# Optimization experiments

Hardware: AMD Instinct MI355X
Metric: run time of the kernel (lower is better)

The kernel has to match this reference:

```python
import jax, jax.numpy as jnp
import numpy as np

N_HEADS = 16


def setup_inputs() -> dict:
    key = jax.random.key(0)
    ks = jax.random.split(key, 5)
    B, T, C = 4, 2048, 1024
    x = jax.random.normal(ks[0], (B, T, C), dtype=jnp.float32)
    w_qkv = jax.random.normal(ks[1], (C, 3 * C), dtype=jnp.float32) * (1.0 / np.sqrt(C))
    b_qkv = jnp.zeros((3 * C,), dtype=jnp.float32)
    w_proj = jax.random.normal(ks[2], (C, C), dtype=jnp.float32) * (1.0 / np.sqrt(C))
    b_proj = jnp.zeros((C,), dtype=jnp.float32)
    return {"x": x, "w_qkv": w_qkv, "b_qkv": b_qkv, "w_proj": w_proj, "b_proj": b_proj}


def reference(x, w_qkv, b_qkv, w_proj, b_proj):
    B, T, C = x.shape
    H = N_HEADS
    D = C // H
    scale = 1.0 / np.sqrt(D).astype(np.float32)
    qkv = x @ w_qkv + b_qkv                      # [B,T,3C]
    qkv = qkv.reshape(B, T, 3, H, D)
    q, k, v = [jnp.transpose(qkv[:, :, i], (0, 2, 1, 3)) for i in range(3)]  # [B,H,T,D]
    attn = jnp.einsum('bhqd,bhkd->bhqk', q, k) * scale
    causal = jnp.tril(jnp.ones((T, T), dtype=bool))
    attn = jnp.where(causal[None, None], attn, -jnp.inf)
    attn = jax.nn.softmax(attn, axis=-1)
    out = jnp.einsum('bhqk,bhkd->bhqd', attn, v)  # [B,H,T,D]
    out = jnp.transpose(out, (0, 2, 1, 3)).reshape(B, T, C)
    return out @ w_proj + b_proj
```

## Files before the change

kernel.cpp:

```cpp
#include <hip/hip_runtime.h>
#include <cstdint>

typedef unsigned short u16;
typedef uint32_t u32;
typedef __attribute__((ext_vector_type(8))) short bf16x8;
typedef __attribute__((ext_vector_type(4))) short bf16x4;
typedef __attribute__((ext_vector_type(4))) float f32x4;

#define NB 4
#define NT 2048
#define NC 1024
#define NH 16
#define ND 64
#define NM (NB*NT)
#define N3C (3*NC)
#define NQT (NT/64)

#define QSCALE 0.18033688011112042f

static __device__ __forceinline__ u16 f2bf(float f){
  union { float f; uint32_t u; } v; v.f = f;
  return (u16)((v.u + 0x7fffu + ((v.u >> 16) & 1u)) >> 16);
}

static __device__ __forceinline__ void gld_lds16(void* lds, const void* g){
  auto lp = reinterpret_cast<__attribute__((address_space(3))) uint32_t*>(
      reinterpret_cast<uintptr_t>(lds));
  auto gp = reinterpret_cast<__attribute__((address_space(1))) uint32_t*>(
      reinterpret_cast<uintptr_t>(g));
  __builtin_amdgcn_global_load_lds(gp, lp, 16, 0, 0);
}

static __device__ __forceinline__ f32x4 mfma16(bf16x4 a, bf16x4 b, f32x4 c){
#if __has_builtin(__builtin_amdgcn_mfma_f32_16x16x16bf16_1k)
  return __builtin_amdgcn_mfma_f32_16x16x16bf16_1k(a, b, c, 0, 0, 0);
#else
  asm("v_mfma_f32_16x16x16_bf16 %0, %1, %2, %0" : "+v"(c) : "v"(a), "v"(b));
  return c;
#endif
}

__global__ __launch_bounds__(256) void k_cast(const float* __restrict__ in,
                                              u16* __restrict__ out){
  const int i = (blockIdx.x * 256 + threadIdx.x) * 4;
  const float4 vv = *reinterpret_cast<const float4*>(in + i);
  union { u16 s[4]; uint64_t u; } pk;
  pk.s[0] = f2bf(vv.x); pk.s[1] = f2bf(vv.y);
  pk.s[2] = f2bf(vv.z); pk.s[3] = f2bf(vv.w);
  *reinterpret_cast<uint64_t*>(out + i) = pk.u;
}

__global__ __launch_bounds__(256) void k_transpose_cast(const float* __restrict__ in,
                                                        u16* __restrict__ out,
                                                        int R, int Cc){
  __shared__ float tile[32][33];
  const int bx = blockIdx.x * 32, by = blockIdx.y * 32;
  const int tx = threadIdx.x, ty = threadIdx.y;
#pragma unroll
  for (int i = 0; i < 32; i += 8)
    tile[ty + i][tx] = in[(size_t)(by + ty + i) * Cc + bx + tx];
  __syncthreads();
#pragma unroll
  for (int i = 0; i < 32; i += 8)
    out[(size_t)(bx + ty + i) * R + by + tx] = f2bf(tile[tx][ty + i]);
}

static __device__ __forceinline__ void gemm_mainloop(
    const u16* __restrict__ A, const u16* __restrict__ Bt, int K,
    int m0, int n0, u16* As, u16* Bs, f32x4 acc[4][4])
{
  const int tid = threadIdx.x;
  const int wave = tid >> 6, lane = tid & 63;
  const int wm = wave >> 1, wn = wave & 1;
  const int o0 = tid * 8, o1 = o0 + 2048;
  const u16* Ag0 = A  + (size_t)(m0 + (o0 >> 5)) * K + (o0 & 31);
  const u16* Ag1 = A  + (size_t)(m0 + (o1 >> 5)) * K + (o1 & 31);
  const u16* Bg0 = Bt + (size_t)(n0 + (o0 >> 5)) * K + (o0 & 31);
  const u16* Bg1 = Bt + (size_t)(n0 + (o1 >> 5)) * K + (o1 & 31);
  u16* AsW = As + wave * 512;
  u16* BsW = Bs + wave * 512;
  const int kb = (lane >> 4) * 8, rl = lane & 15;

  for (int kt = 0; kt < K; kt += 32){
    gld_lds16(AsW,        Ag0 + kt);
    gld_lds16(AsW + 2048, Ag1 + kt);
    gld_lds16(BsW,        Bg0 + kt);
    gld_lds16(BsW + 2048, Bg1 + kt);
    __syncthreads();
    bf16x8 af[4], bfr[4];
#pragma unroll
    for (int i = 0; i < 4; i++){
      af[i]  = *reinterpret_cast<const bf16x8*>(&As[(wm * 64 + i * 16 + rl) * 32 + kb]);
      bfr[i] = *reinterpret_cast<const bf16x8*>(&Bs[(wn * 64 + i * 16 + rl) * 32 + kb]);
    }
#pragma unroll
    for (int i = 0; i < 4; i++)
#pragma unroll
      for (int j = 0; j < 4; j++)
        acc[i][j] = __builtin_amdgcn_mfma_f32_16x16x32_bf16(af[i], bfr[j], acc[i][j], 0, 0, 0);
    __syncthreads();
  }
}

__global__ __launch_bounds__(256) void k_gemm_qkv(
    const u16* __restrict__ A, const u16* __restrict__ Bt,
    const float* __restrict__ bias,
    u16* __restrict__ qo, u16* __restrict__ ko, u16* __restrict__ vo)
{
  __shared__ u16 As[128 * 32], Bs[128 * 32];
  f32x4 acc[4][4] = {};
  const int m0 = blockIdx.y * 128, n0 = blockIdx.x * 128;
  gemm_mainloop(A, Bt, NC, m0, n0, As, Bs, acc);

  const int tid = threadIdx.x;
  const int wave = tid >> 6, lane = tid & 63;
  const int wm = wave >> 1, wn = wave & 1;
  const int rl = lane & 15, rg = lane >> 4;
  const int which = n0 >> 10;
  if (which == 2){
#pragma unroll
    for (int j = 0; j < 4; j++){
      const int n = n0 + wn * 64 + j * 16 + rl;
      const int cc = n & 1023;
      const int h = cc >> 6, d = cc & 63;
      const float bb = bias[n];
#pragma unroll
      for (int i = 0; i < 4; i++){
        const int mb = m0 + wm * 64 + i * 16 + rg * 4;
        const int b = mb >> 11, t0 = mb & 2047;
        const size_t bhb = ((size_t)(b * NH + h)) * NT * ND;
        union { u16 s[4]; uint64_t u; } pk4;
#pragma unroll
        for (int r = 0; r < 4; r++) pk4.s[r] = f2bf(acc[i][j][r] + bb);
        *reinterpret_cast<uint64_t*>(
          &vo[bhb + (size_t)(t0 >> 6) * 4096 + d * 64 + ((((t0 >> 2) & 15) ^ (d & 7)) << 2)]) = pk4.u;
      }
    }
  } else {
#pragma unroll
    for (int j = 0; j < 4; j++){
      const int n = n0 + wn * 64 + j * 16 + rl;
      const int cc = n & 1023;
      const int h = cc >> 6, d = cc & 63;
      const float bb = bias[n];
#pragma unroll
      for (int i = 0; i < 4; i++){
#pragma unroll
        for (int r = 0; r < 4; r++){
          const int m = m0 + wm * 64 + i * 16 + rg * 4 + r;
          const int b = m >> 11, t = m & 2047;
          const size_t bhb = ((size_t)(b * NH + h)) * NT * ND;
          const float val = acc[i][j][r] + bb;
          if (which == 0){
            qo[bhb + (size_t)t * ND + d] = f2bf(val * QSCALE);
          } else {
            ko[bhb + (size_t)(t >> 6) * 4096 + (t & 63) * 64 + (d ^ ((t & 7) << 3))] = f2bf(val);
          }
        }
      }
    }
  }
}

__global__ __launch_bounds__(256) void k_gemm_proj(
    const u16* __restrict__ A, const u16* __restrict__ Bt,
    const float* __restrict__ bias, float* __restrict__ out)
{
  __shared__ u16 As[128 * 32], Bs[128 * 32];
  f32x4 acc[4][4] = {};
  const int m0 = blockIdx.y * 128, n0 = blockIdx.x * 128;
  gemm_mainloop(A, Bt, NC, m0, n0, As, Bs, acc);

  const int tid = threadIdx.x;
  const int wave = tid >> 6, lane = tid & 63;
  const int wm = wave >> 1, wn = wave & 1;
  const int rl = lane & 15, rg = lane >> 4;
#pragma unroll
  for (int i = 0; i < 4; i++){
#pragma unroll
    for (int r = 0; r < 4; r++){
      const int m = m0 + wm * 64 + i * 16 + rg * 4 + r;
#pragma unroll
      for (int j = 0; j < 4; j++){
        const int n = n0 + wn * 64 + j * 16 + rl;
        out[(size_t)m * NC + n] = acc[i][j][r] + bias[n];
      }
    }
  }
}

static __device__ __forceinline__ void flash_one(
    int qt, const u16* __restrict__ q, const u16* __restrict__ kb,
    const u16* __restrict__ vb, u16* __restrict__ ao, int bh,
    u16 (*Ks)[4096], u16 (*Vt)[4096])
{
  const int tid = threadIdx.x, wave = tid >> 6, lane = tid & 63;
  const int cl = lane & 15, g = lane >> 4;
  const int c0 = wave * 2;
  const size_t base = (size_t)bh * NT * ND;
  const u16* kg0 = kb + base;
  const u16* vg0 = vb + base;

  bf16x8 qf0, qf1;
  {
    const u16* qrow = q + base + (size_t)(qt * 64 + wave * 16 + cl) * ND;
    qf0 = *reinterpret_cast<const bf16x8*>(qrow + g * 8);
    qf1 = *reinterpret_cast<const bf16x8*>(qrow + 32 + g * 8);
  }
  asm volatile("" : "+v"(qf0), "+v"(qf1));

  f32x4 o[4] = {};
  float mrun = -1e30f, lrun = 0.f;
  const int n = qt + 1;

  gld_lds16(&Ks[0][(c0    ) * 512], kg0 + (c0    ) * 512 + lane * 8);
  gld_lds16(&Ks[0][(c0 + 1) * 512], kg0 + (c0 + 1) * 512 + lane * 8);
  gld_lds16(&Vt[0][(c0    ) * 512], vg0 + (c0    ) * 512 + lane * 8);
  gld_lds16(&Vt[0][(c0 + 1) * 512], vg0 + (c0 + 1) * 512 + lane * 8);

  for (int t = 0; t < n; ++t){
    const int cur = t & 1, nxt = cur ^ 1;
    if (t + 1 < n){
      const u16* kg = kg0 + (size_t)(t + 1) * 4096;
      const u16* vg = vg0 + (size_t)(t + 1) * 4096;
      gld_lds16(&Ks[nxt][(c0    ) * 512], kg + (c0    ) * 512 + lane * 8);
      gld_lds16(&Ks[nxt][(c0 + 1) * 512], kg + (c0 + 1) * 512 + lane * 8);
      gld_lds16(&Vt[nxt][(c0    ) * 512], vg + (c0    ) * 512 + lane * 8);
      gld_lds16(&Vt[nxt][(c0 + 1) * 512], vg + (c0 + 1) * 512 + lane * 8);
      asm volatile("s_waitcnt vmcnt(4)" ::: "memory");
    } else {
      asm volatile("s_waitcnt vmcnt(0)" ::: "memory");
    }
    __builtin_amdgcn_sched_barrier(0);
    __builtin_amdgcn_s_barrier();

    const u16* KsC = Ks[cur];
    const u16* VtC = Vt[cur];
    f32x4 s[4];
    __builtin_amdgcn_s_setprio(1);
#pragma unroll
    for (int nf = 0; nf < 4; nf++){
      const int kj = nf * 16 + cl;
      const u16* krow = &KsC[kj * 64];
      const bf16x8 kf0 = *reinterpret_cast<const bf16x8*>(&krow[((0 + g) ^ (kj & 7)) * 8]);
      const bf16x8 kf1 = *reinterpret_cast<const bf16x8*>(&krow[((4 + g) ^ (kj & 7)) * 8]);
      f32x4 a = {};
      a = __builtin_amdgcn_mfma_f32_16x16x32_bf16(kf0, qf0, a, 0, 0, 0);
      a = __builtin_amdgcn_mfma_f32_16x16x32_bf16(kf1, qf1, a, 0, 0, 0);
      s[nf] = a;
    }
    __builtin_amdgcn_s_setprio(0);

    if (t == qt){
      const int qrl = wave * 16 + cl;
#pragma unroll
      for (int nf = 0; nf < 4; nf++)
#pragma unroll
        for (int r = 0; r < 4; r++)
          if (nf * 16 + g * 4 + r > qrl) s[nf][r] = -3e38f;
    }

    float rmax = -3e38f;
#pragma unroll
    for (int nf = 0; nf < 4; nf++)
#pragma unroll
      for (int r = 0; r < 4; r++) rmax = fmaxf(rmax, s[nf][r]);
    rmax = fmaxf(rmax, __shfl_xor(rmax, 16));
    rmax = fmaxf(rmax, __shfl_xor(rmax, 32));
    const float mnew = fmaxf(mrun, rmax);
    const float alpha = exp2f(mrun - mnew);
    mrun = mnew;
    float rs = 0.f;
#pragma unroll
    for (int nf = 0; nf < 4; nf++)
#pragma unroll
      for (int r = 0; r < 4; r++){
        s[nf][r] = exp2f(s[nf][r] - mnew);
        rs += s[nf][r];
      }
    rs += __shfl_xor(rs, 16);
    rs += __shfl_xor(rs, 32);
    lrun = lrun * alpha + rs;

    const float a0 = __shfl(alpha, g * 4 + 0);
    const float a1 = __shfl(alpha, g * 4 + 1);
    const float a2 = __shfl(alpha, g * 4 + 2);
    const float a3 = __shfl(alpha, g * 4 + 3);
#pragma unroll
    for (int fo = 0; fo < 4; fo++){
      o[fo][0] *= a0; o[fo][1] *= a1; o[fo][2] *= a2; o[fo][3] *= a3;
    }

    u32 pk[4][2];
#pragma unroll
    for (int nf = 0; nf < 4; nf++){
      asm("v_cvt_pk_bf16_f32 %0, %1, %2" : "=v"(pk[nf][0]) : "v"(s[nf][0]), "v"(s[nf][1]));
      asm("v_cvt_pk_bf16_f32 %0, %1, %2" : "=v"(pk[nf][1]) : "v"(s[nf][2]), "v"(s[nf][3]));
    }

    __builtin_amdgcn_s_setprio(1);
#pragma unroll
    for (int nf = 0; nf < 4; nf++){
      union { u32 u[2]; bf16x4 v; } pa;
      pa.u[0] = pk[nf][0]; pa.u[1] = pk[nf][1];
#pragma unroll
      for (int fo = 0; fo < 4; fo++){
        const int d = fo * 16 + cl;
        const bf16x4 vf = *reinterpret_cast<const bf16x4*>(
            &VtC[d * 64 + (((nf * 4 + g) ^ (d & 7)) << 2)]);
        o[fo] = mfma16(pa.v, vf, o[fo]);
      }
    }
    __builtin_amdgcn_s_setprio(0);

    asm volatile("s_waitcnt lgkmcnt(0)" ::: "memory");
    __builtin_amdgcn_sched_barrier(0);
    __builtin_amdgcn_s_barrier();
  }

  float linv[4];
#pragma unroll
  for (int r = 0; r < 4; r++) linv[r] = 1.0f / __shfl(lrun, g * 4 + r);
  const int b = bh >> 4, h = bh & 15;
#pragma unroll
  for (int fo = 0; fo < 4; fo++){
#pragma unroll
    for (int r = 0; r < 4; r++){
      const int t = qt * 64 + wave * 16 + g * 4 + r;
      const int c = h * 64 + fo * 16 + cl;
      ao[((size_t)b * NT + t) * NC + c] = f2bf(o[fo][r] * linv[r]);
    }
  }
}

__global__ __launch_bounds__(256) void k_flash(
    const u16* __restrict__ q, const u16* __restrict__ k,
    const u16* __restrict__ v, u16* __restrict__ ao)
{
  __shared__ u16 Ks[2][4096];
  __shared__ u16 Vt[2][4096];
  const int px = blockIdx.x, bh = blockIdx.y;
  flash_one(px,           q, k, v, ao, bh, Ks, Vt);
  __builtin_amdgcn_s_barrier();
  flash_one(NQT - 1 - px, q, k, v, ao, bh, Ks, Vt);
}

extern "C" void kernel_launch(void* const* d_in, const int* in_sizes, int n_in,
                              void* d_out, int out_size, void* d_ws, size_t ws_size,
                              hipStream_t stream){
  const float* x      = (const float*)d_in[0];
  const float* w_qkv  = (const float*)d_in[1];
  const float* b_qkv  = (const float*)d_in[2];
  const float* w_proj = (const float*)d_in[3];
  const float* b_proj = (const float*)d_in[4];
  float* out = (float*)d_out;

  u16* ws = (u16*)d_ws;
  u16* xb     = ws;
  u16* qb     = ws + 8388608;
  u16* kb     = ws + 16777216;
  u16* vb     = ws + 25165824;
  u16* aob    = ws + 33554432;
  u16* wqkvT  = ws + 41943040;
  u16* wprojT = ws + 45088768;

  k_cast<<<8388608 / 1024, 256, 0, stream>>>(x, xb);
  k_transpose_cast<<<dim3(N3C / 32, NC / 32), dim3(32, 8), 0, stream>>>(w_qkv, wqkvT, NC, N3C);
  k_transpose_cast<<<dim3(NC / 32, NC / 32), dim3(32, 8), 0, stream>>>(w_proj, wprojT, NC, NC);
  k_gemm_qkv<<<dim3(N3C / 128, NM / 128), 256, 0, stream>>>(xb, wqkvT, b_qkv, qb, kb, vb);
  k_flash<<<dim3(NQT / 2, NB * NH), 256, 0, stream>>>(qb, kb, vb, aob);
  k_gemm_proj<<<dim3(NC / 128, NM / 128), 256, 0, stream>>>(aob, wprojT, b_proj, out);
}
```

Measured before the change: 228.7 us.

## Process paired query tiles in one KV sweep and skip rescale when max stable

Each flash block previously handled its two causal-balanced query tiles in two separate passes over K/V. Now both tiles share a single pass: each K/V chunk is loaded into LDS once and used for both query tiles, the shorter tile stopping at its diagonal. This removes the duplicated K/V global loads and barriers. The softmax also skips the alpha rescale of the output accumulator unless the running max grows by more than a threshold, a lazy-rescale trick that trades a small numeric-range margin for fewer multiplies. Holding two sets of accumulators raises register pressure, which may lower occupancy.

```diff
diff --git a/kernel.cpp b/kernel.cpp
--- a/kernel.cpp
+++ b/kernel.cpp
@@ -189,38 +189,131 @@
   }
 }
 
-static __device__ __forceinline__ void flash_one(
-    int qt, const u16* __restrict__ q, const u16* __restrict__ kb,
-    const u16* __restrict__ vb, u16* __restrict__ ao, int bh,
-    u16 (*Ks)[4096], u16 (*Vt)[4096])
-{
+static __device__ __forceinline__ void qkt(const u16* __restrict__ KsC,
+                                           bf16x8 qf0, bf16x8 qf1,
+                                           int cl, int g, f32x4 s[4])
+{
+  __builtin_amdgcn_s_setprio(1);
+#pragma unroll
+  for (int nf = 0; nf < 4; nf++){
+    const int kj = nf * 16 + cl;
+    const u16* krow = &KsC[kj * 64];
+    const bf16x8 kf0 = *reinterpret_cast<const bf16x8*>(&krow[((0 + g) ^ (kj & 7)) * 8]);
+    const bf16x8 kf1 = *reinterpret_cast<const bf16x8*>(&krow[((4 + g) ^ (kj & 7)) * 8]);
+    f32x4 a = {};
+    a = __builtin_amdgcn_mfma_f32_16x16x32_bf16(kf0, qf0, a, 0, 0, 0);
+    a = __builtin_amdgcn_mfma_f32_16x16x32_bf16(kf1, qf1, a, 0, 0, 0);
+    s[nf] = a;
+  }
+  __builtin_amdgcn_s_setprio(0);
+}
+
+static __device__ __forceinline__ void maskdiag(f32x4 s[4], int wave, int cl, int g){
+  const int qrl = wave * 16 + cl;
+#pragma unroll
+  for (int nf = 0; nf < 4; nf++)
+#pragma unroll
+    for (int r = 0; r < 4; r++)
+      if (nf * 16 + g * 4 + r > qrl) s[nf][r] = -3e38f;
+}
+
+static __device__ __forceinline__ void sm_pv(
+    f32x4 s[4], f32x4 o[4], float& mrun, float& lrun,
+    const u16* __restrict__ VtC, int cl, int g)
+{
+  float rmax = -3e38f;
+#pragma unroll
+  for (int nf = 0; nf < 4; nf++)
+#pragma unroll
+    for (int r = 0; r < 4; r++) rmax = fmaxf(rmax, s[nf][r]);
+  rmax = fmaxf(rmax, __shfl_xor(rmax, 16));
+  rmax = fmaxf(rmax, __shfl_xor(rmax, 32));
+  if (!__all(rmax <= mrun + 8.0f)){
+    const float mnew = fmaxf(mrun, rmax);
+    const float alpha = exp2f(mrun - mnew);
+    mrun = mnew;
+    lrun *= alpha;
+    const float a0 = __shfl(alpha, g * 4 + 0);
+    const float a1 = __shfl(alpha, g * 4 + 1);
+    const float a2 = __shfl(alpha, g * 4 + 2);
+    const float a3 = __shfl(alpha, g * 4 + 3);
+#pragma unroll
+    for (int fo = 0; fo < 4; fo++){
+      o[fo][0] *= a0; o[fo][1] *= a1; o[fo][2] *= a2; o[fo][3] *= a3;
+    }
+  }
+  float rs = 0.f;
+#pragma unroll
+  for (int nf = 0; nf < 4; nf++)
+#pragma unroll
+    for (int r = 0; r < 4; r++){
+      s[nf][r] = exp2f(s[nf][r] - mrun);
+      rs += s[nf][r];
+    }
+  rs += __shfl_xor(rs, 16);
+  rs += __shfl_xor(rs, 32);
+  lrun += rs;
+
+  u32 pk[4][2];
+#pragma unroll
+  for (int nf = 0; nf < 4; nf++){
+    asm("v_cvt_pk_bf16_f32 %0, %1, %2" : "=v"(pk[nf][0]) : "v"(s[nf][0]), "v"(s[nf][1]));
+    asm("v_cvt_pk_bf16_f32 %0, %1, %2" : "=v"(pk[nf][1]) : "v"(s[nf][2]), "v"(s[nf][3]));
+  }
+  __builtin_amdgcn_s_setprio(1);
+#pragma unroll
+  for (int nf = 0; nf < 4; nf++){
+    union { u32 u[2]; bf16x4 v; } pa;
+    pa.u[0] = pk[nf][0]; pa.u[1] = pk[nf][1];
+#pragma unroll
+    for (int fo = 0; fo < 4; fo++){
+      const int d = fo * 16 + cl;
+      const bf16x4 vf = *reinterpret_cast<const bf16x4*>(
+          &VtC[d * 64 + (((nf * 4 + g) ^ (d & 7)) << 2)]);
+      o[fo] = mfma16(pa.v, vf, o[fo]);
+    }
+  }
+  __builtin_amdgcn_s_setprio(0);
+}
+
+__global__ __launch_bounds__(256) void k_flash(
+    const u16* __restrict__ q, const u16* __restrict__ k,
+    const u16* __restrict__ v, u16* __restrict__ ao)
+{
+  __shared__ u16 Ks[2][4096];
+  __shared__ u16 Vt[2][4096];
   const int tid = threadIdx.x, wave = tid >> 6, lane = tid & 63;
   const int cl = lane & 15, g = lane >> 4;
   const int c0 = wave * 2;
+  const int px = blockIdx.x, bh = blockIdx.y;
+  const int qt1 = px, qt2 = NQT - 1 - px;
+  const int ntot = qt2 + 1;
   const size_t base = (size_t)bh * NT * ND;
-  const u16* kg0 = kb + base;
-  const u16* vg0 = vb + base;
-
-  bf16x8 qf0, qf1;
+  const u16* kg0 = k + base;
+  const u16* vg0 = v + base;
+
+  bf16x8 q1f0, q1f1, q2f0, q2f1;
   {
-    const u16* qrow = q + base + (size_t)(qt * 64 + wave * 16 + cl) * ND;
-    qf0 = *reinterpret_cast<const bf16x8*>(qrow + g * 8);
-    qf1 = *reinterpret_cast<const bf16x8*>(qrow + 32 + g * 8);
-  }
-  asm volatile("" : "+v"(qf0), "+v"(qf1));
-
-  f32x4 o[4] = {};
-  float mrun = -1e30f, lrun = 0.f;
-  const int n = qt + 1;
+    const u16* qr1 = q + base + (size_t)(qt1 * 64 + wave * 16 + cl) * ND;
+    q1f0 = *reinterpret_cast<const bf16x8*>(qr1 + g * 8);
+    q1f1 = *reinterpret_cast<const bf16x8*>(qr1 + 32 + g * 8);
+    const u16* qr2 = q + base + (size_t)(qt2 * 64 + wave * 16 + cl) * ND;
+    q2f0 = *reinterpret_cast<const bf16x8*>(qr2 + g * 8);
+    q2f1 = *reinterpret_cast<const bf16x8*>(qr2 + 32 + g * 8);
+  }
+  asm volatile("" : "+v"(q1f0), "+v"(q1f1), "+v"(q2f0), "+v"(q2f1));
+
+  f32x4 o1[4] = {}, o2[4] = {};
+  float m1 = -1e30f, l1 = 0.f, m2 = -1e30f, l2 = 0.f;
 
   gld_lds16(&Ks[0][(c0    ) * 512], kg0 + (c0    ) * 512 + lane * 8);
   gld_lds16(&Ks[0][(c0 + 1) * 512], kg0 + (c0 + 1) * 512 + lane * 8);
   gld_lds16(&Vt[0][(c0    ) * 512], vg0 + (c0    ) * 512 + lane * 8);
   gld_lds16(&Vt[0][(c0 + 1) * 512], vg0 + (c0 + 1) * 512 + lane * 8);
 
-  for (int t = 0; t < n; ++t){
+  for (int t = 0; t < ntot; ++t){
     const int cur = t & 1, nxt = cur ^ 1;
-    if (t + 1 < n){
+    if (t + 1 < ntot){
       const u16* kg = kg0 + (size_t)(t + 1) * 4096;
       const u16* vg = vg0 + (size_t)(t + 1) * 4096;
       gld_lds16(&Ks[nxt][(c0    ) * 512], kg + (c0    ) * 512 + lane * 8);
@@ -236,113 +329,43 @@
 
     const u16* KsC = Ks[cur];
     const u16* VtC = Vt[cur];
-    f32x4 s[4];
-    __builtin_amdgcn_s_setprio(1);
-#pragma unroll
-    for (int nf = 0; nf < 4; nf++){
-      const int kj = nf * 16 + cl;
-      const u16* krow = &KsC[kj * 64];
-      const bf16x8 kf0 = *reinterpret_cast<const bf16x8*>(&krow[((0 + g) ^ (kj & 7)) * 8]);
-      const bf16x8 kf1 = *reinterpret_cast<const bf16x8*>(&krow[((4 + g) ^ (kj & 7)) * 8]);
-      f32x4 a = {};
-      a = __builtin_amdgcn_mfma_f32_16x16x32_bf16(kf0, qf0, a, 0, 0, 0);
-      a = __builtin_amdgcn_mfma_f32_16x16x32_bf16(kf1, qf1, a, 0, 0, 0);
-      s[nf] = a;
-    }
-    __builtin_amdgcn_s_setprio(0);
-
-    if (t == qt){
-      const int qrl = wave * 16 + cl;
-#pragma unroll
-      for (int nf = 0; nf < 4; nf++)
-#pragma unroll
-        for (int r = 0; r < 4; r++)
-          if (nf * 16 + g * 4 + r > qrl) s[nf][r] = -3e38f;
-    }
-
-    float rmax = -3e38f;
-#pragma unroll
-    for (int nf = 0; nf < 4; nf++)
-#pragma unroll
-      for (int r = 0; r < 4; r++) rmax = fmaxf(rmax, s[nf][r]);
-    rmax = fmaxf(rmax, __shfl_xor(rmax, 16));
-    rmax = fmaxf(rmax, __shfl_xor(rmax, 32));
-    const float mnew = fmaxf(mrun, rmax);
-    const float alpha = exp2f(mrun - mnew);
-    mrun = mnew;
-    float rs = 0.f;
-#pragma unroll
-    for (int nf = 0; nf < 4; nf++)
-#pragma unroll
-      for (int r = 0; r < 4; r++){
-        s[nf][r] = exp2f(s[nf][r] - mnew);
-        rs += s[nf][r];
-      }
-    rs += __shfl_xor(rs, 16);
-    rs += __shfl_xor(rs, 32);
-    lrun = lrun * alpha + rs;
-
-    const float a0 = __shfl(alpha, g * 4 + 0);
-    const float a1 = __shfl(alpha, g * 4 + 1);
-    const float a2 = __shfl(alpha, g * 4 + 2);
-    const float a3 = __shfl(alpha, g * 4 + 3);
-#pragma unroll
-    for (int fo = 0; fo < 4; fo++){
-      o[fo][0] *= a0; o[fo][1] *= a1; o[fo][2] *= a2; o[fo][3] *= a3;
-    }
-
-    u32 pk[4][2];
-#pragma unroll
-    for (int nf = 0; nf < 4; nf++){
-      asm("v_cvt_pk_bf16_f32 %0, %1, %2" : "=v"(pk[nf][0]) : "v"(s[nf][0]), "v"(s[nf][1]));
-      asm("v_cvt_pk_bf16_f32 %0, %1, %2" : "=v"(pk[nf][1]) : "v"(s[nf][2]), "v"(s[nf][3]));
-    }
-
-    __builtin_amdgcn_s_setprio(1);
-#pragma unroll
-    for (int nf = 0; nf < 4; nf++){
-      union { u32 u[2]; bf16x4 v; } pa;
-      pa.u[0] = pk[nf][0]; pa.u[1] = pk[nf][1];
-#pragma unroll
-      for (int fo = 0; fo < 4; fo++){
-        const int d = fo * 16 + cl;
-        const bf16x4 vf = *reinterpret_cast<const bf16x4*>(
-            &VtC[d * 64 + (((nf * 4 + g) ^ (d & 7)) << 2)]);
-        o[fo] = mfma16(pa.v, vf, o[fo]);
-      }
-    }
-    __builtin_amdgcn_s_setprio(0);
+
+    {
+      f32x4 s[4];
+      qkt(KsC, q2f0, q2f1, cl, g, s);
+      if (t == qt2) maskdiag(s, wave, cl, g);
+      sm_pv(s, o2, m2, l2, VtC, cl, g);
+    }
+    if (t <= qt1){
+      f32x4 s[4];
+      qkt(KsC, q1f0, q1f1, cl, g, s);
+      if (t == qt1) maskdiag(s, wave, cl, g);
+      sm_pv(s, o1, m1, l1, VtC, cl, g);
+    }
 
     asm volatile("s_waitcnt lgkmcnt(0)" ::: "memory");
     __builtin_amdgcn_sched_barrier(0);
     __builtin_amdgcn_s_barrier();
   }
 
-  float linv[4];
-#pragma unroll
-  for (int r = 0; r < 4; r++) linv[r] = 1.0f / __shfl(lrun, g * 4 + r);
+  float li1[4], li2[4];
+#pragma unroll
+  for (int r = 0; r < 4; r++){
+    li1[r] = 1.0f / __shfl(l1, g * 4 + r);
+    li2[r] = 1.0f / __shfl(l2, g * 4 + r);
+  }
   const int b = bh >> 4, h = bh & 15;
 #pragma unroll
   for (int fo = 0; fo < 4; fo++){
 #pragma unroll
     for (int r = 0; r < 4; r++){
-      const int t = qt * 64 + wave * 16 + g * 4 + r;
       const int c = h * 64 + fo * 16 + cl;
-      ao[((size_t)b * NT + t) * NC + c] = f2bf(o[fo][r] * linv[r]);
-    }
-  }
-}
-
-__global__ __launch_bounds__(256) void k_flash(
-    const u16* __restrict__ q, const u16* __restrict__ k,
-    const u16* __restrict__ v, u16* __restrict__ ao)
-{
-  __shared__ u16 Ks[2][4096];
-  __shared__ u16 Vt[2][4096];
-  const int px = blockIdx.x, bh = blockIdx.y;
-  flash_one(px,           q, k, v, ao, bh, Ks, Vt);
-  __builtin_amdgcn_s_barrier();
-  flash_one(NQT - 1 - px, q, k, v, ao, bh, Ks, Vt);
+      const int t1 = qt1 * 64 + wave * 16 + g * 4 + r;
+      ao[((size_t)b * NT + t1) * NC + c] = f2bf(o1[fo][r] * li1[r]);
+      const int t2 = qt2 * 64 + wave * 16 + g * 4 + r;
+      ao[((size_t)b * NT + t2) * NC + c] = f2bf(o2[fo][r] * li2[r]);
+    }
+  }
 }
 
 extern "C" void kernel_launch(void* const* d_in, const int* in_sizes, int n_in,
```

After: 223.2 us. -2.4%, faster.

## Rewrite flash attention with 32x32 MFMA, shared KV stream for paired query tiles

Applied to the files above, without the earlier changes.

The flash kernel moves from 16x16 MFMA tiles to 32x32x16 bf16 MFMA, with each wave owning 32 query rows. Each block now processes its two causal-balanced 128-row query blocks together while streaming a single K/V pass, so K/V tiles staged into LDS are reused by both query sets. The V layout written by the QKV GEMM changes to an 8-element swizzle to match the new fragment loads. It also adds permlane32 swaps to build the P operand and a lazy rescale that skips the alpha correction unless the row max grows by more than 8. The trade-off is higher register pressure from two sets of accumulators and Q fragments, and a grid halved to 8x64 blocks.

```diff
diff --git a/kernel.cpp b/kernel.cpp
--- a/kernel.cpp
+++ b/kernel.cpp
@@ -4,8 +4,8 @@
 typedef unsigned short u16;
 typedef uint32_t u32;
 typedef __attribute__((ext_vector_type(8))) short bf16x8;
-typedef __attribute__((ext_vector_type(4))) short bf16x4;
 typedef __attribute__((ext_vector_type(4))) float f32x4;
+typedef __attribute__((ext_vector_type(16))) float f32x16;
 
 #define NB 4
 #define NT 2048
@@ -14,7 +14,6 @@
 #define ND 64
 #define NM (NB*NT)
 #define N3C (3*NC)
-#define NQT (NT/64)
 
 #define QSCALE 0.18033688011112042f
 
@@ -31,13 +30,8 @@
   __builtin_amdgcn_global_load_lds(gp, lp, 16, 0, 0);
 }
 
-static __device__ __forceinline__ f32x4 mfma16(bf16x4 a, bf16x4 b, f32x4 c){
-#if __has_builtin(__builtin_amdgcn_mfma_f32_16x16x16bf16_1k)
-  return __builtin_amdgcn_mfma_f32_16x16x16bf16_1k(a, b, c, 0, 0, 0);
-#else
-  asm("v_mfma_f32_16x16x16_bf16 %0, %1, %2, %0" : "+v"(c) : "v"(a), "v"(b));
-  return c;
-#endif
+static __device__ __forceinline__ f32x16 mfma32(bf16x8 a, bf16x8 b, f32x16 c){
+  return __builtin_amdgcn_mfma_f32_32x32x16_bf16(a, b, c, 0, 0, 0);
 }
 
 __global__ __launch_bounds__(256) void k_cast(const float* __restrict__ in,
@@ -133,7 +127,8 @@
 #pragma unroll
         for (int r = 0; r < 4; r++) pk4.s[r] = f2bf(acc[i][j][r] + bb);
         *reinterpret_cast<uint64_t*>(
-          &vo[bhb + (size_t)(t0 >> 6) * 4096 + d * 64 + ((((t0 >> 2) & 15) ^ (d & 7)) << 2)]) = pk4.u;
+          &vo[bhb + (size_t)(t0 >> 6) * 4096 + d * 64 +
+              ((((t0 >> 3) & 7) ^ (d & 7)) << 3) + (t0 & 7)]) = pk4.u;
       }
     }
   } else {
@@ -189,44 +184,160 @@
   }
 }
 
-static __device__ __forceinline__ void flash_one(
-    int qt, const u16* __restrict__ q, const u16* __restrict__ kb,
-    const u16* __restrict__ vb, u16* __restrict__ ao, int bh,
-    u16 (*Ks)[4096], u16 (*Vt)[4096])
-{
+static __device__ __forceinline__ void upd32(
+    const u16* __restrict__ Kc, const u16* __restrict__ Vc,
+    const bf16x8* qf, f32x16& o0, f32x16& o1,
+    float& mrun, float& lrun, int kbase, int qglob, bool domask,
+    int hi, int l31, int l7)
+{
+  f32x16 s0 = {}, s1 = {};
+  __builtin_amdgcn_s_setprio(1);
+#pragma unroll
+  for (int ds = 0; ds < 4; ds++){
+    const int sw = ((ds * 2 + hi) ^ l7) << 3;
+    const bf16x8 kf0 = *reinterpret_cast<const bf16x8*>(&Kc[l31 * 64 + sw]);
+    const bf16x8 kf1 = *reinterpret_cast<const bf16x8*>(&Kc[(32 + l31) * 64 + sw]);
+    s0 = mfma32(kf0, qf[ds], s0);
+    s1 = mfma32(kf1, qf[ds], s1);
+  }
+  __builtin_amdgcn_s_setprio(0);
+
+  if (domask){
+#pragma unroll
+    for (int r = 0; r < 16; r++){
+      const int krow = (r & 3) + 8 * (r >> 2) + 4 * hi;
+      if (kbase + krow      > qglob) s0[r] = -3e38f;
+      if (kbase + 32 + krow > qglob) s1[r] = -3e38f;
+    }
+  }
+
+  float ta[8];
+#pragma unroll
+  for (int i = 0; i < 8; i++)
+    ta[i] = fmaxf(fmaxf(s0[2*i], s0[2*i+1]), fmaxf(s1[2*i], s1[2*i+1]));
+  float rmax = fmaxf(fmaxf(fmaxf(ta[0], ta[1]), fmaxf(ta[2], ta[3])),
+                     fmaxf(fmaxf(ta[4], ta[5]), fmaxf(ta[6], ta[7])));
+  rmax = fmaxf(rmax, __shfl_xor(rmax, 32));
+
+  if (!__all(rmax <= mrun + 8.0f)){
+    const float mnew = fmaxf(mrun, rmax);
+    const float alpha = exp2f(mrun - mnew);
+    mrun = mnew;
+    lrun *= alpha;
+    o0 *= alpha;
+    o1 *= alpha;
+  }
+#pragma unroll
+  for (int r = 0; r < 16; r++){
+    s0[r] = exp2f(s0[r] - mrun);
+    s1[r] = exp2f(s1[r] - mrun);
+  }
+  float sa[8];
+#pragma unroll
+  for (int i = 0; i < 8; i++)
+    sa[i] = (s0[2*i] + s0[2*i+1]) + (s1[2*i] + s1[2*i+1]);
+  float rs = ((sa[0] + sa[1]) + (sa[2] + sa[3])) + ((sa[4] + sa[5]) + (sa[6] + sa[7]));
+  rs += __shfl_xor(rs, 32);
+  lrun += rs;
+
+#pragma unroll
+  for (int ks = 0; ks < 4; ks++){
+    u32 wa, wb, wc, wd;
+    if (ks < 2){
+      const int rb = ks * 8;
+      asm("v_cvt_pk_bf16_f32 %0, %1, %2" : "=v"(wa) : "v"(s0[rb+0]), "v"(s0[rb+1]));
+      asm("v_cvt_pk_bf16_f32 %0, %1, %2" : "=v"(wb) : "v"(s0[rb+2]), "v"(s0[rb+3]));
+      asm("v_cvt_pk_bf16_f32 %0, %1, %2" : "=v"(wc) : "v"(s0[rb+4]), "v"(s0[rb+5]));
+      asm("v_cvt_pk_bf16_f32 %0, %1, %2" : "=v"(wd) : "v"(s0[rb+6]), "v"(s0[rb+7]));
+    } else {
+      const int rb = (ks - 2) * 8;
+      asm("v_cvt_pk_bf16_f32 %0, %1, %2" : "=v"(wa) : "v"(s1[rb+0]), "v"(s1[rb+1]));
+      asm("v_cvt_pk_bf16_f32 %0, %1, %2" : "=v"(wb) : "v"(s1[rb+2]), "v"(s1[rb+3]));
+      asm("v_cvt_pk_bf16_f32 %0, %1, %2" : "=v"(wc) : "v"(s1[rb+4]), "v"(s1[rb+5]));
+      asm("v_cvt_pk_bf16_f32 %0, %1, %2" : "=v"(wd) : "v"(s1[rb+6]), "v"(s1[rb+7]));
+    }
+    asm("v_permlane32_swap_b32 %0, %1" : "+v"(wa), "+v"(wc));
+    asm("v_permlane32_swap_b32 %0, %1" : "+v"(wb), "+v"(wd));
+    union { u32 u[4]; bf16x8 v; } pf;
+    pf.u[0] = wa; pf.u[1] = wb; pf.u[2] = wc; pf.u[3] = wd;
+    const int sw = ((ks * 2 + hi) ^ l7) << 3;
+    const bf16x8 vf0 = *reinterpret_cast<const bf16x8*>(&Vc[l31 * 64 + sw]);
+    const bf16x8 vf1 = *reinterpret_cast<const bf16x8*>(&Vc[(32 + l31) * 64 + sw]);
+    __builtin_amdgcn_s_setprio(1);
+    o0 = mfma32(vf0, pf.v, o0);
+    o1 = mfma32(vf1, pf.v, o1);
+    __builtin_amdgcn_s_setprio(0);
+  }
+}
+
+static __device__ __forceinline__ void epi32(u16* __restrict__ ao, size_t rowb,
+                                             float li, const f32x16& oa,
+                                             const f32x16& ob, int hi){
+#pragma unroll
+  for (int dsub = 0; dsub < 2; dsub++){
+    const f32x16& ov = dsub ? ob : oa;
+#pragma unroll
+    for (int rg = 0; rg < 4; rg++){
+      union { u16 s4[4]; uint64_t u; } pk4;
+#pragma unroll
+      for (int q4 = 0; q4 < 4; q4++) pk4.s4[q4] = f2bf(ov[rg * 4 + q4] * li);
+      *reinterpret_cast<uint64_t*>(&ao[rowb + dsub * 32 + rg * 8 + hi * 4]) = pk4.u;
+    }
+  }
+}
+
+__global__ __launch_bounds__(256) void k_flash(
+    const u16* __restrict__ q, const u16* __restrict__ k,
+    const u16* __restrict__ v, u16* __restrict__ ao)
+{
+  __shared__ u16 Ks[2][4096];
+  __shared__ u16 Vt[2][4096];
   const int tid = threadIdx.x, wave = tid >> 6, lane = tid & 63;
-  const int cl = lane & 15, g = lane >> 4;
+  const int l31 = lane & 31, hi = lane >> 5, l7 = lane & 7;
   const int c0 = wave * 2;
+  const int px = blockIdx.x, bh = blockIdx.y;
+  const int qb1 = px, qb2 = 15 - px;
+  const int npt = 2 * qb2 + 2;
+  const int tmax1 = 2 * qb1 + (wave >> 1);
+  const int tmax2 = 2 * qb2 + (wave >> 1);
   const size_t base = (size_t)bh * NT * ND;
-  const u16* kg0 = kb + base;
-  const u16* vg0 = vb + base;
-
-  bf16x8 qf0, qf1;
+  const u16* kg0 = k + base;
+  const u16* vg0 = v + base;
+  const int qg1 = qb1 * 128 + wave * 32 + l31;
+  const int qg2 = qb2 * 128 + wave * 32 + l31;
+
+  bf16x8 q1[4], q2[4];
   {
-    const u16* qrow = q + base + (size_t)(qt * 64 + wave * 16 + cl) * ND;
-    qf0 = *reinterpret_cast<const bf16x8*>(qrow + g * 8);
-    qf1 = *reinterpret_cast<const bf16x8*>(qrow + 32 + g * 8);
-  }
-  asm volatile("" : "+v"(qf0), "+v"(qf1));
-
-  f32x4 o[4] = {};
-  float mrun = -1e30f, lrun = 0.f;
-  const int n = qt + 1;
-
-  gld_lds16(&Ks[0][(c0    ) * 512], kg0 + (c0    ) * 512 + lane * 8);
-  gld_lds16(&Ks[0][(c0 + 1) * 512], kg0 + (c0 + 1) * 512 + lane * 8);
-  gld_lds16(&Vt[0][(c0    ) * 512], vg0 + (c0    ) * 512 + lane * 8);
-  gld_lds16(&Vt[0][(c0 + 1) * 512], vg0 + (c0 + 1) * 512 + lane * 8);
-
-  for (int t = 0; t < n; ++t){
+    const u16* p1 = q + base + (size_t)qg1 * 64 + hi * 8;
+    const u16* p2 = q + base + (size_t)qg2 * 64 + hi * 8;
+#pragma unroll
+    for (int ds = 0; ds < 4; ds++){
+      q1[ds] = *reinterpret_cast<const bf16x8*>(p1 + ds * 16);
+      q2[ds] = *reinterpret_cast<const bf16x8*>(p2 + ds * 16);
+    }
+  }
+  asm volatile("" : "+v"(q1[0]), "+v"(q1[1]), "+v"(q1[2]), "+v"(q1[3]),
+                    "+v"(q2[0]), "+v"(q2[1]), "+v"(q2[2]), "+v"(q2[3]));
+
+  f32x16 o1a = {}, o1b = {}, o2a = {}, o2b = {};
+  float m1 = -1e30f, l1 = 0.f, m2 = -1e30f, l2 = 0.f;
+
+#define STAGE(BUF, T)                                                          \
+  {                                                                            \
+    const u16* kg = kg0 + (size_t)(T) * 4096;                                  \
+    const u16* vg = vg0 + (size_t)(T) * 4096;                                  \
+    gld_lds16(&Ks[BUF][(c0    ) * 512], kg + (c0    ) * 512 + lane * 8);       \
+    gld_lds16(&Ks[BUF][(c0 + 1) * 512], kg + (c0 + 1) * 512 + lane * 8);       \
+    gld_lds16(&Vt[BUF][(c0    ) * 512], vg + (c0    ) * 512 + lane * 8);       \
+    gld_lds16(&Vt[BUF][(c0 + 1) * 512], vg + (c0 + 1) * 512 + lane * 8);       \
+  }
+
+  STAGE(0, 0);
+
+  for (int t = 0; t < npt; ++t){
     const int cur = t & 1, nxt = cur ^ 1;
-    if (t + 1 < n){
-      const u16* kg = kg0 + (size_t)(t + 1) * 4096;
-      const u16* vg = vg0 + (size_t)(t + 1) * 4096;
-      gld_lds16(&Ks[nxt][(c0    ) * 512], kg + (c0    ) * 512 + lane * 8);
-      gld_lds16(&Ks[nxt][(c0 + 1) * 512], kg + (c0 + 1) * 512 + lane * 8);
-      gld_lds16(&Vt[nxt][(c0    ) * 512], vg + (c0    ) * 512 + lane * 8);
-      gld_lds16(&Vt[nxt][(c0 + 1) * 512], vg + (c0 + 1) * 512 + lane * 8);
+    if (t + 1 < npt){
+      STAGE(nxt, t + 1);
       asm volatile("s_waitcnt vmcnt(4)" ::: "memory");
     } else {
       asm volatile("s_waitcnt vmcnt(0)" ::: "memory");
@@ -234,115 +345,22 @@
     __builtin_amdgcn_sched_barrier(0);
     __builtin_amdgcn_s_barrier();
 
-    const u16* KsC = Ks[cur];
-    const u16* VtC = Vt[cur];
-    f32x4 s[4];
-    __builtin_amdgcn_s_setprio(1);
-#pragma unroll
-    for (int nf = 0; nf < 4; nf++){
-      const int kj = nf * 16 + cl;
-      const u16* krow = &KsC[kj * 64];
-      const bf16x8 kf0 = *reinterpret_cast<const bf16x8*>(&krow[((0 + g) ^ (kj & 7)) * 8]);
-      const bf16x8 kf1 = *reinterpret_cast<const bf16x8*>(&krow[((4 + g) ^ (kj & 7)) * 8]);
-      f32x4 a = {};
-      a = __builtin_amdgcn_mfma_f32_16x16x32_bf16(kf0, qf0, a, 0, 0, 0);
-      a = __builtin_amdgcn_mfma_f32_16x16x32_bf16(kf1, qf1, a, 0, 0, 0);
-      s[nf] = a;
-    }
-    __builtin_amdgcn_s_setprio(0);
-
-    if (t == qt){
-      const int qrl = wave * 16 + cl;
-#pragma unroll
-      for (int nf = 0; nf < 4; nf++)
-#pragma unroll
-        for (int r = 0; r < 4; r++)
-          if (nf * 16 + g * 4 + r > qrl) s[nf][r] = -3e38f;
-    }
-
-    float rmax = -3e38f;
-#pragma unroll
-    for (int nf = 0; nf < 4; nf++)
-#pragma unroll
-      for (int r = 0; r < 4; r++) rmax = fmaxf(rmax, s[nf][r]);
-    rmax = fmaxf(rmax, __shfl_xor(rmax, 16));
-    rmax = fmaxf(rmax, __shfl_xor(rmax, 32));
-    const float mnew = fmaxf(mrun, rmax);
-    const float alpha = exp2f(mrun - mnew);
-    mrun = mnew;
-    float rs = 0.f;
-#pragma unroll
-    for (int nf = 0; nf < 4; nf++)
-#pragma unroll
-      for (int r = 0; r < 4; r++){
-        s[nf][r] = exp2f(s[nf][r] - mnew);
-        rs += s[nf][r];
-      }
-    rs += __shfl_xor(rs, 16);
-    rs += __shfl_xor(rs, 32);
-    lrun = lrun * alpha + rs;
-
-    const float a0 = __shfl(alpha, g * 4 + 0);
-    const float a1 = __shfl(alpha, g * 4 + 1);
-    const float a2 = __shfl(alpha, g * 4 + 2);
-    const float a3 = __shfl(alpha, g * 4 + 3);
-#pragma unroll
-    for (int fo = 0; fo < 4; fo++){
-      o[fo][0] *= a0; o[fo][1] *= a1; o[fo][2] *= a2; o[fo][3] *= a3;
-    }
-
-    u32 pk[4][2];
-#pragma unroll
-    for (int nf = 0; nf < 4; nf++){
-      asm("v_cvt_pk_bf16_f32 %0, %1, %2" : "=v"(pk[nf][0]) : "v"(s[nf][0]), "v"(s[nf][1]));
-      asm("v_cvt_pk_bf16_f32 %0, %1, %2" : "=v"(pk[nf][1]) : "v"(s[nf][2]), "v"(s[nf][3]));
-    }
-
-    __builtin_amdgcn_s_setprio(1);
-#pragma unroll
-    for (int nf = 0; nf < 4; nf++){
-      union { u32 u[2]; bf16x4 v; } pa;
-      pa.u[0] = pk[nf][0]; pa.u[1] = pk[nf][1];
-#pragma unroll
-      for (int fo = 0; fo < 4; fo++){
-        const int d = fo * 16 + cl;
-        const bf16x4 vf = *reinterpret_cast<const bf16x4*>(
-            &VtC[d * 64 + (((nf * 4 + g) ^ (d & 7)) << 2)]);
-        o[fo] = mfma16(pa.v, vf, o[fo]);
-      }
-    }
-    __builtin_amdgcn_s_setprio(0);
+    const u16* Kc = Ks[cur];
+    const u16* Vc = Vt[cur];
+    if (t <= tmax2)
+      upd32(Kc, Vc, q2, o2a, o2b, m2, l2, t * 64, qg2, t == tmax2, hi, l31, l7);
+    if (t <= tmax1)
+      upd32(Kc, Vc, q1, o1a, o1b, m1, l1, t * 64, qg1, t == tmax1, hi, l31, l7);
 
     asm volatile("s_waitcnt lgkmcnt(0)" ::: "memory");
     __builtin_amdgcn_sched_barrier(0);
     __builtin_amdgcn_s_barrier();
   }
-
-  float linv[4];
-#pragma unroll
-  for (int r = 0; r < 4; r++) linv[r] = 1.0f / __shfl(lrun, g * 4 + r);
+#undef STAGE
+
   const int b = bh >> 4, h = bh & 15;
-#pragma unroll
-  for (int fo = 0; fo < 4; fo++){
-#pragma unroll
-    for (int r = 0; r < 4; r++){
-      const int t = qt * 64 + wave * 16 + g * 4 + r;
-      const int c = h * 64 + fo * 16 + cl;
-      ao[((size_t)b * NT + t) * NC + c] = f2bf(o[fo][r] * linv[r]);
-    }
-  }
-}
-
-__global__ __launch_bounds__(256) void k_flash(
-    const u16* __restrict__ q, const u16* __restrict__ k,
-    const u16* __restrict__ v, u16* __restrict__ ao)
-{
-  __shared__ u16 Ks[2][4096];
-  __shared__ u16 Vt[2][4096];
-  const int px = blockIdx.x, bh = blockIdx.y;
-  flash_one(px,           q, k, v, ao, bh, Ks, Vt);
-  __builtin_amdgcn_s_barrier();
-  flash_one(NQT - 1 - px, q, k, v, ao, bh, Ks, Vt);
+  epi32(ao, ((size_t)b * NT + qg1) * NC + h * 64, 1.0f / l1, o1a, o1b, hi);
+  epi32(ao, ((size_t)b * NT + qg2) * NC + h * 64, 1.0f / l2, o2a, o2b, hi);
 }
 
 extern "C" void kernel_launch(void* const* d_in, const int* in_sizes, int n_in,
@@ -368,6 +386,6 @@
   k_transpose_cast<<<dim3(N3C / 32, NC / 32), dim3(32, 8), 0, stream>>>(w_qkv, wqkvT, NC, N3C);
   k_transpose_cast<<<dim3(NC / 32, NC / 32), dim3(32, 8), 0, stream>>>(w_proj, wprojT, NC, NC);
   k_gemm_qkv<<<dim3(N3C / 128, NM / 128), 256, 0, stream>>>(xb, wqkvT, b_qkv, qb, kb, vb);
-  k_flash<<<dim3(NQT / 2, NB * NH), 256, 0, stream>>>(qb, kb, vb, aob);
+  k_flash<<<dim3(8, NB * NH), 256, 0, stream>>>(qb, kb, vb, aob);
   k_gemm_proj<<<dim3(NC / 128, NM / 128), 256, 0, stream>>>(aob, wprojT, b_proj, out);
 }
```

Result: slower. 247.1 us (+8.1%).
